# Performance work log

Measured on AMD Instinct MI355X. Metric: run time of the kernel, lower is better.

The kernel has to match this reference:

```python
import jax, jax.numpy as jnp
import numpy as np

B, S, D, H = 8, 1024, 768, 12
E = D // H  # head_size = 64
EPS = 1e-5


def _ln(x, g, b):
    mu = jnp.mean(x, axis=-1, keepdims=True)
    var = jnp.mean(jnp.square(x - mu), axis=-1, keepdims=True)
    return (x - mu) * jax.lax.rsqrt(var + EPS) * g + b


def setup_inputs() -> dict:
    key = jax.random.key(0)
    ks = jax.random.split(key, 16)
    w = lambda k, shape: jax.random.normal(k, shape, dtype=jnp.float32) * 0.02
    return {
        "x": jax.random.normal(ks[0], (B, S, D), dtype=jnp.float32),
        "ln1_g": jnp.ones((D,), jnp.float32),
        "ln1_b": jnp.zeros((D,), jnp.float32),
        "Wq": w(ks[1], (H, D, E)),
        "bq": w(ks[2], (H, E)),
        "Wv": w(ks[3], (H, D, E)),
        "bv": w(ks[4], (H, E)),
        "Wo": w(ks[5], (H * E, D)),
        "bo": w(ks[6], (D,)),
        "ln2_g": jnp.ones((D,), jnp.float32),
        "ln2_b": jnp.zeros((D,), jnp.float32),
        "W1": w(ks[7], (D, 4 * D)),
        "b1": w(ks[8], (4 * D,)),
        "W2": w(ks[9], (4 * D, D)),
        "b2": w(ks[10], (D,)),
    }


def reference(x, ln1_g, ln1_b, Wq, bq, Wv, bv, Wo, bo, ln2_g, ln2_b, W1, b1, W2, b2):
    d_k = x.shape[-1]
    h = _ln(x, ln1_g, ln1_b)
    # Faithful quirk: keys use the QUERY projection (k = self.query(x) in source).
    q = jnp.einsum('bsd,hde->bhse', h, Wq) + bq[None, :, None, :]
    k = q  # same projection, same input -> identical tensor
    v = jnp.einsum('bsd,hde->bhse', h, Wv) + bv[None, :, None, :]
    # Faithful quirk: scale uses full d_k, not head_size.
    scores = jnp.einsum('bhse,bhte->bhst', q, k) * (d_k ** -0.5)
    prob = jax.nn.softmax(scores, axis=-1)
    o = jnp.einsum('bhst,bhte->bhse', prob, v)  # [B,H,S,E]
    o = o.transpose(0, 2, 1, 3).reshape(x.shape[0], x.shape[1], -1)  # concat heads
    x = x + o @ Wo + bo
    h2 = _ln(x, ln2_g, ln2_b)
    mlp = jax.nn.gelu(h2 @ W1 + b1, approximate=False) @ W2 + b2
    return x + mlp
```

## Files before the change

### kernel.cpp

```cpp
#include <hip/hip_runtime.h>
#include <stdint.h>


typedef __attribute__((ext_vector_type(8))) short s8v;
typedef __attribute__((ext_vector_type(4))) float f32x4;
typedef __attribute__((ext_vector_type(4))) unsigned short us4v;

__device__ __forceinline__ unsigned short f2b(float f) {
  union { float f; unsigned u; } v; v.f = f;
  unsigned r = v.u + 0x7FFFu + ((v.u >> 16) & 1u);
  return (unsigned short)(r >> 16);
}

__device__ __forceinline__ void g2l16(const unsigned short* g, unsigned short* l) {
  __builtin_amdgcn_global_load_lds(
      (const __attribute__((address_space(1))) unsigned int*)g,
      (__attribute__((address_space(3))) unsigned int*)l, 16, 0, 0);
}

#define QSCALE 0.22816534f

__global__ __launch_bounds__(256) void repack_kernel(
    const float* __restrict__ Wq, const float* __restrict__ bq,
    const float* __restrict__ Wv, const float* __restrict__ bv,
    const float* __restrict__ Wo, const float* __restrict__ W1,
    const float* __restrict__ W2,
    unsigned short* __restrict__ Wqv_t, float* __restrict__ bias_qv,
    unsigned short* __restrict__ Wo_t, unsigned short* __restrict__ W1_t,
    unsigned short* __restrict__ W2_t)
{
  int i = blockIdx.x * 256 + threadIdx.x;
  if (i < 1536 * 768) {
    int n = i / 768, d = i % 768;
    float val;
    if (n < 768) { int h = n >> 6, e = n & 63; val = Wq[(h * 768 + d) * 64 + e] * QSCALE; }
    else { int c = n - 768; int h = c >> 6, e = c & 63; val = Wv[(h * 768 + d) * 64 + e]; }
    Wqv_t[i] = f2b(val);
  }
  if (i < 1536) bias_qv[i] = (i < 768) ? bq[i] * QSCALE : bv[i - 768];
  if (i < 768 * 768)  { int n = i / 768,  k = i % 768;  Wo_t[i] = f2b(Wo[k * 768  + n]); }
  if (i < 3072 * 768) { int n = i / 768,  k = i % 768;  W1_t[i] = f2b(W1[k * 3072 + n]); }
  if (i < 768 * 3072) { int n = i / 3072, k = i % 3072; W2_t[i] = f2b(W2[k * 768  + n]); }
}

__global__ __launch_bounds__(256) void ln_kernel(
    const float* __restrict__ x, const float* __restrict__ g,
    const float* __restrict__ b, unsigned short* __restrict__ out)
{
  __shared__ float red[4], red2[4];
  int row = blockIdx.x, t = threadIdx.x;
  const float* xr = x + (size_t)row * 768;
  float v0 = xr[t], v1 = xr[t + 256], v2 = xr[t + 512];
  float s = v0 + v1 + v2;
  #pragma unroll
  for (int m = 32; m; m >>= 1) s += __shfl_xor(s, m);
  if ((t & 63) == 0) red[t >> 6] = s;
  __syncthreads();
  float mean = (red[0] + red[1] + red[2] + red[3]) * (1.f / 768.f);
  float d0 = v0 - mean, d1 = v1 - mean, d2 = v2 - mean;
  float vs = d0 * d0 + d1 * d1 + d2 * d2;
  #pragma unroll
  for (int m = 32; m; m >>= 1) vs += __shfl_xor(vs, m);
  if ((t & 63) == 0) red2[t >> 6] = vs;
  __syncthreads();
  float var = (red2[0] + red2[1] + red2[2] + red2[3]) * (1.f / 768.f);
  float rs = rsqrtf(var + 1e-5f);
  unsigned short* o = out + (size_t)row * 768;
  o[t]       = f2b(d0 * rs * g[t]       + b[t]);
  o[t + 256] = f2b(d1 * rs * g[t + 256] + b[t + 256]);
  o[t + 512] = f2b(d2 * rs * g[t + 512] + b[t + 512]);
}

template<int EPI, int N, int K>
__global__ __launch_bounds__(512, 4) void gemm128(
    const unsigned short* __restrict__ A, const unsigned short* __restrict__ Bt,
    const float* __restrict__ bias,
    const float* resid, float* out_f32,
    unsigned short* __restrict__ out_bf,
    unsigned short* __restrict__ q_out, unsigned short* __restrict__ vt_out)
{
  __shared__ __align__(16) unsigned short As_[2][8192];
  __shared__ __align__(16) unsigned short Bs_[2][8192];
  constexpr int NTN = N >> 7;
  constexpr int NT = K >> 6;
  int bid = blockIdx.x;
  int q8 = gridDim.x >> 3;
  int sb = (bid & 7) * q8 + (bid >> 3);
  int m0 = (sb / NTN) << 7, n0 = (sb % NTN) << 7;
  int t = threadIdx.x, lane = t & 63, w = t >> 6;
  int l15 = lane & 15, lg = lane >> 4;
  int wm = (w >> 2) << 6;
  int wn = (w & 3) << 5;
  int lrow = lane >> 3;
  int lxor = ((lane & 7) ^ lrow) << 3;
  const unsigned short* Abase = A + (size_t)m0 * K;
  const unsigned short* Bbase = Bt + (size_t)n0 * K;

  auto stage = [&](int buf, int tile) {
    int k0 = tile << 6;
    #pragma unroll
    for (int j = 0; j < 2; ++j) {
      int row = j * 64 + w * 8 + lrow;
      int doff = (j * 512 + w * 64) * 8;
      g2l16(&Abase[(size_t)row * K + k0 + lxor], &As_[buf][doff]);
      g2l16(&Bbase[(size_t)row * K + k0 + lxor], &Bs_[buf][doff]);
    }
  };

  f32x4 acc[4][2] = {};
  stage(0, 0);
  asm volatile("s_waitcnt vmcnt(0)" ::: "memory");
  __builtin_amdgcn_sched_barrier(0);
  __builtin_amdgcn_s_barrier();

  int cswz = (l15 & 7) << 3;
  for (int tt = 0; tt < NT; ++tt) {
    int cur = tt & 1;
    if (tt + 1 < NT) {
      stage(cur ^ 1, tt + 1);
      asm volatile("s_waitcnt vmcnt(4)" ::: "memory");
    } else {
      asm volatile("s_waitcnt vmcnt(0)" ::: "memory");
    }
    __builtin_amdgcn_sched_barrier(0);
    __builtin_amdgcn_s_barrier();
    __builtin_amdgcn_sched_barrier(0);
    const unsigned short* Ac = &As_[cur][0];
    const unsigned short* Bc = &Bs_[cur][0];
    #pragma unroll
    for (int kk = 0; kk < 2; ++kk) {
      s8v a[4], b[2];
      int col = (kk * 32 + lg * 8) ^ cswz;
      #pragma unroll
      for (int i = 0; i < 4; ++i)
        a[i] = *(const s8v*)&Ac[(wm + i * 16 + l15) * 64 + col];
      #pragma unroll
      for (int i = 0; i < 2; ++i)
        b[i] = *(const s8v*)&Bc[(wn + i * 16 + l15) * 64 + col];
      __builtin_amdgcn_s_setprio(1);
      #pragma unroll
      for (int mi = 0; mi < 4; ++mi)
        #pragma unroll
        for (int ni = 0; ni < 2; ++ni)
          acc[mi][ni] = __builtin_amdgcn_mfma_f32_16x16x32_bf16(a[mi], b[ni], acc[mi][ni], 0, 0, 0);
      __builtin_amdgcn_s_setprio(0);
    }
    if (tt + 1 < NT) {
      __builtin_amdgcn_sched_barrier(0);
      __builtin_amdgcn_s_barrier();
      __builtin_amdgcn_sched_barrier(0);
    }
  }
  #pragma unroll
  for (int mi = 0; mi < 4; ++mi) {
    #pragma unroll
    for (int ni = 0; ni < 2; ++ni) {
      int col = n0 + wn + ni * 16 + l15;
      float bs = bias[col];
      #pragma unroll
      for (int r = 0; r < 4; ++r) {
        int row = m0 + wm + mi * 16 + lg * 4 + r;
        float v = acc[mi][ni][r] + bs;
        if (EPI == 1) {
          out_f32[(size_t)row * N + col] = resid[(size_t)row * N + col] + v;
        } else if (EPI == 2) {
          float v2 = v * v;
          float z = v * fmaf(-0.10294202f, v2, -2.302026f);
          float e; asm("v_exp_f32 %0, %1" : "=v"(e) : "v"(z));
          float rcp; asm("v_rcp_f32 %0, %1" : "=v"(rcp) : "v"(e + 1.0f));
          out_bf[(size_t)row * N + col] = f2b(v * rcp);
        } else {
          if (col < 768) {
            q_out[(size_t)row * 768 + col] = f2b(v);
          } else {
            int c = col - 768; int hh = c >> 6, e = c & 63;
            int bb = row >> 10, s = row & 1023;
            vt_out[(((size_t)(bb * 12 + hh)) * 64 + e) * 1024 + s] = f2b(v);
          }
        }
      }
    }
  }
}

__global__ __launch_bounds__(256) void attn_kernel(
    const unsigned short* __restrict__ qk,
    const unsigned short* __restrict__ vt,
    unsigned short* __restrict__ o)
{
  __shared__ __align__(16) unsigned short Qs[128 * 64];
  __shared__ __align__(16) unsigned short Ks[2][64 * 64];
  __shared__ __align__(16) unsigned short Vs[2][64 * 64];
  __shared__ __align__(16) unsigned short Ps[128 * 64];
  int bid = blockIdx.x;
  int xcd = bid & 7, idx = bid >> 3;
  int bh = xcd * 12 + (idx >> 3), qt = idx & 7;
  int b = bh / 12, h = bh % 12;
  int t = threadIdx.x, lane = t & 63, w = t >> 6;
  int l15 = lane & 15, lg = lane >> 4;
  int wq0 = w << 5;
  size_t qrow0 = (size_t)b * 1024 + qt * 128;
  size_t krow0 = (size_t)b * 1024;
  size_t vbase = ((size_t)bh) * 64 * 1024;

  int srow = t >> 3;
  int scsw = ((t & 7) << 3) ^ ((srow & 7) << 3);
  const unsigned short* qsrc = &qk[(qrow0 + srow) * 768 + h * 64 + scsw];
  const unsigned short* ksrc = &qk[(krow0 + srow) * 768 + h * 64 + scsw];
  const unsigned short* vsrc = &vt[vbase + (size_t)srow * 1024 + scsw];

  #pragma unroll
  for (int j = 0; j < 4; ++j)
    g2l16(qsrc + (size_t)j * 32 * 768, &Qs[(j * 256 + w * 64) * 8]);
  #pragma unroll
  for (int j = 0; j < 2; ++j) {
    g2l16(ksrc + (size_t)j * 32 * 768, &Ks[0][(j * 256 + w * 64) * 8]);
    g2l16(vsrc + (size_t)j * 32 * 1024, &Vs[0][(j * 256 + w * 64) * 8]);
  }
  asm volatile("s_waitcnt vmcnt(0)" ::: "memory");
  __builtin_amdgcn_s_barrier();

  f32x4 oacc[4][2] = {};
  float lsum[2] = {0.f, 0.f};
  int cswz = (l15 & 7) << 3;

  for (int kt = 0; kt < 16; ++kt) {
    int buf = kt & 1;
    if (kt < 15) {
      const unsigned short* kp = ksrc + (size_t)(kt + 1) * 64 * 768;
      const unsigned short* vp = vsrc + (kt + 1) * 64;
      #pragma unroll
      for (int j = 0; j < 2; ++j) {
        g2l16(kp + (size_t)j * 32 * 768, &Ks[buf ^ 1][(j * 256 + w * 64) * 8]);
        g2l16(vp + (size_t)j * 32 * 1024, &Vs[buf ^ 1][(j * 256 + w * 64) * 8]);
      }
    }
    const unsigned short* Kb = Ks[buf];
    const unsigned short* Vb = Vs[buf];
    f32x4 st[4][2] = {};
    #pragma unroll
    for (int kk = 0; kk < 2; ++kk) {
      int col = (kk * 32 + lg * 8) ^ cswz;
      s8v a[4], bq2[2];
      #pragma unroll
      for (int i = 0; i < 4; ++i) a[i] = *(const s8v*)&Kb[(i * 16 + l15) * 64 + col];
      #pragma unroll
      for (int i = 0; i < 2; ++i) bq2[i] = *(const s8v*)&Qs[(wq0 + i * 16 + l15) * 64 + col];
      #pragma unroll
      for (int mi = 0; mi < 4; ++mi)
        #pragma unroll
        for (int ni = 0; ni < 2; ++ni)
          st[mi][ni] = __builtin_amdgcn_mfma_f32_16x16x32_bf16(a[mi], bq2[ni], st[mi][ni], 0, 0, 0);
    }
    #pragma unroll
    for (int ni = 0; ni < 2; ++ni) {
      int prow = (wq0 + ni * 16 + l15) * 64;
      #pragma unroll
      for (int mi = 0; mi < 4; ++mi) {
        float p0, p1, p2, p3;
        asm("v_exp_f32 %0, %1" : "=v"(p0) : "v"(st[mi][ni][0]));
        asm("v_exp_f32 %0, %1" : "=v"(p1) : "v"(st[mi][ni][1]));
        asm("v_exp_f32 %0, %1" : "=v"(p2) : "v"(st[mi][ni][2]));
        asm("v_exp_f32 %0, %1" : "=v"(p3) : "v"(st[mi][ni][3]));
        lsum[ni] += (p0 + p1) + (p2 + p3);
        unsigned lo, hi;
        asm("v_cvt_pk_bf16_f32 %0, %1, %2" : "=v"(lo) : "v"(p0), "v"(p1));
        asm("v_cvt_pk_bf16_f32 %0, %1, %2" : "=v"(hi) : "v"(p2), "v"(p3));
        unsigned long long pk = (unsigned long long)lo | ((unsigned long long)hi << 32);
        *(unsigned long long*)&Ps[prow + ((mi * 16 + lg * 4) ^ cswz)] = pk;
      }
    }
    #pragma unroll
    for (int kk = 0; kk < 2; ++kk) {
      int col = (kk * 32 + lg * 8) ^ cswz;
      s8v a[4], bp[2];
      #pragma unroll
      for (int i = 0; i < 4; ++i) a[i] = *(const s8v*)&Vb[(i * 16 + l15) * 64 + col];
      #pragma unroll
      for (int i = 0; i < 2; ++i) bp[i] = *(const s8v*)&Ps[(wq0 + i * 16 + l15) * 64 + col];
      #pragma unroll
      for (int ei = 0; ei < 4; ++ei)
        #pragma unroll
        for (int ni = 0; ni < 2; ++ni)
          oacc[ei][ni] = __builtin_amdgcn_mfma_f32_16x16x32_bf16(a[ei], bp[ni], oacc[ei][ni], 0, 0, 0);
    }
    asm volatile("s_waitcnt vmcnt(0)" ::: "memory");
    __builtin_amdgcn_s_barrier();
  }
  #pragma unroll
  for (int ni = 0; ni < 2; ++ni) {
    float s = lsum[ni];
    s += __shfl_xor(s, 16);
    s += __shfl_xor(s, 32);
    float inv = 1.f / s;
    int q = wq0 + ni * 16 + l15;
    size_t obase = (qrow0 + q) * 768 + h * 64;
    #pragma unroll
    for (int ei = 0; ei < 4; ++ei) {
      us4v ov;
      #pragma unroll
      for (int r = 0; r < 4; ++r) ov[r] = f2b(oacc[ei][ni][r] * inv);
      *(us4v*)&o[obase + ei * 16 + lg * 4] = ov;
    }
  }
}

extern "C" void kernel_launch(void* const* d_in, const int* in_sizes, int n_in,
                              void* d_out, int out_size, void* d_ws, size_t ws_size,
                              hipStream_t stream)
{
  const float* x     = (const float*)d_in[0];
  const float* ln1_g = (const float*)d_in[1];
  const float* ln1_b = (const float*)d_in[2];
  const float* Wq    = (const float*)d_in[3];
  const float* bq    = (const float*)d_in[4];
  const float* Wv    = (const float*)d_in[5];
  const float* bv    = (const float*)d_in[6];
  const float* Wo    = (const float*)d_in[7];
  const float* bo    = (const float*)d_in[8];
  const float* ln2_g = (const float*)d_in[9];
  const float* ln2_b = (const float*)d_in[10];
  const float* W1    = (const float*)d_in[11];
  const float* b1    = (const float*)d_in[12];
  const float* W2    = (const float*)d_in[13];
  const float* b2    = (const float*)d_in[14];
  float* out = (float*)d_out;

  char* ws = (char*)d_ws;
  size_t off = 0;
  auto alloc = [&](size_t bytes) -> void* {
    void* p = ws + off; off += (bytes + 255) & ~(size_t)255; return p;
  };
  unsigned short* Wqv_t  = (unsigned short*)alloc(1536ull * 768 * 2);
  float*          bias_qv= (float*)         alloc(1536ull * 4);
  unsigned short* Wo_t   = (unsigned short*)alloc(768ull * 768 * 2);
  unsigned short* W1_t   = (unsigned short*)alloc(3072ull * 768 * 2);
  unsigned short* W2_t   = (unsigned short*)alloc(768ull * 3072 * 2);
  unsigned short* h_bf   = (unsigned short*)alloc(8192ull * 768 * 2);
  unsigned short* q_bf   = (unsigned short*)alloc(8192ull * 768 * 2);
  unsigned short* v_t    = (unsigned short*)alloc(96ull * 64 * 1024 * 2);
  unsigned short* o_bf   = (unsigned short*)alloc(8192ull * 768 * 2);
  unsigned short* h2_bf  = (unsigned short*)alloc(8192ull * 768 * 2);
  unsigned short* m1_bf  = (unsigned short*)alloc(8192ull * 3072 * 2);

  repack_kernel<<<9216, 256, 0, stream>>>(Wq, bq, Wv, bv, Wo, W1, W2,
                                          Wqv_t, bias_qv, Wo_t, W1_t, W2_t);
  ln_kernel<<<8192, 256, 0, stream>>>(x, ln1_g, ln1_b, h_bf);
  gemm128<3, 1536, 768><<<768, 512, 0, stream>>>(h_bf, Wqv_t, bias_qv,
      nullptr, nullptr, nullptr, q_bf, v_t);
  attn_kernel<<<768, 256, 0, stream>>>(q_bf, v_t, o_bf);
  gemm128<1, 768, 768><<<384, 512, 0, stream>>>(o_bf, Wo_t, bo,
      x, out, nullptr, nullptr, nullptr);
  ln_kernel<<<8192, 256, 0, stream>>>(out, ln2_g, ln2_b, h2_bf);
  gemm128<2, 3072, 768><<<1536, 512, 0, stream>>>(h2_bf, W1_t, b1,
      nullptr, nullptr, m1_bf, nullptr, nullptr);
  gemm128<1, 768, 3072><<<384, 512, 0, stream>>>(m1_bf, W2_t, b2,
      out, out, nullptr, nullptr, nullptr);
}
```

Before: 278.3 us.

## Split K across wave pairs in GEMM with LDS reduction of partial accumulators

The 128x128 GEMM now assigns each group of four waves a 64x64 output sub-tile and splits the 64-wide K tile between two wave groups, each handling 32. Each wave loads 4 A and 4 B fragments for 16 MFMAs per tile instead of 4+2 fragments for 8 MFMAs over two k-steps. This raises MFMA-to-LDS-read ratio. After the main loop, the upper four waves write their partial sums into LDS, and the lower four add them and run the epilogue. The cost is doubled accumulator registers, an extra reduction with two barriers, and an epilogue executed by only half the waves.

Result: slower. 299.3 us (median of 2 runs) (+7.5%).

```diff
diff --git a/kernel.cpp b/kernel.cpp
--- a/kernel.cpp
+++ b/kernel.cpp
@@ -79,8 +79,7 @@
     unsigned short* __restrict__ out_bf,
     unsigned short* __restrict__ q_out, unsigned short* __restrict__ vt_out)
 {
-  __shared__ __align__(16) unsigned short As_[2][8192];
-  __shared__ __align__(16) unsigned short Bs_[2][8192];
+  __shared__ __align__(16) unsigned short SMEM[2][16384];
   constexpr int NTN = N >> 7;
   constexpr int NT = K >> 6;
   int bid = blockIdx.x;
@@ -89,8 +88,8 @@
   int m0 = (sb / NTN) << 7, n0 = (sb % NTN) << 7;
   int t = threadIdx.x, lane = t & 63, w = t >> 6;
   int l15 = lane & 15, lg = lane >> 4;
-  int wm = (w >> 2) << 6;
-  int wn = (w & 3) << 5;
+  int p = w & 3, kks = w >> 2;
+  int wm = (p >> 1) << 6, wn = (p & 1) << 6;
   int lrow = lane >> 3;
   int lxor = ((lane & 7) ^ lrow) << 3;
   const unsigned short* Abase = A + (size_t)m0 * K;
@@ -102,18 +101,18 @@
     for (int j = 0; j < 2; ++j) {
       int row = j * 64 + w * 8 + lrow;
       int doff = (j * 512 + w * 64) * 8;
-      g2l16(&Abase[(size_t)row * K + k0 + lxor], &As_[buf][doff]);
-      g2l16(&Bbase[(size_t)row * K + k0 + lxor], &Bs_[buf][doff]);
+      g2l16(&Abase[(size_t)row * K + k0 + lxor], &SMEM[buf][doff]);
+      g2l16(&Bbase[(size_t)row * K + k0 + lxor], &SMEM[buf][8192 + doff]);
     }
   };
 
-  f32x4 acc[4][2] = {};
+  f32x4 acc[4][4] = {};
   stage(0, 0);
   asm volatile("s_waitcnt vmcnt(0)" ::: "memory");
   __builtin_amdgcn_sched_barrier(0);
   __builtin_amdgcn_s_barrier();
 
-  int cswz = (l15 & 7) << 3;
+  int col = (kks * 32 + lg * 8) ^ ((l15 & 7) << 3);
   for (int tt = 0; tt < NT; ++tt) {
     int cur = tt & 1;
     if (tt + 1 < NT) {
@@ -125,57 +124,72 @@
     __builtin_amdgcn_sched_barrier(0);
     __builtin_amdgcn_s_barrier();
     __builtin_amdgcn_sched_barrier(0);
-    const unsigned short* Ac = &As_[cur][0];
-    const unsigned short* Bc = &Bs_[cur][0];
-    #pragma unroll
-    for (int kk = 0; kk < 2; ++kk) {
-      s8v a[4], b[2];
-      int col = (kk * 32 + lg * 8) ^ cswz;
-      #pragma unroll
-      for (int i = 0; i < 4; ++i)
-        a[i] = *(const s8v*)&Ac[(wm + i * 16 + l15) * 64 + col];
-      #pragma unroll
-      for (int i = 0; i < 2; ++i)
-        b[i] = *(const s8v*)&Bc[(wn + i * 16 + l15) * 64 + col];
-      __builtin_amdgcn_s_setprio(1);
-      #pragma unroll
-      for (int mi = 0; mi < 4; ++mi)
-        #pragma unroll
-        for (int ni = 0; ni < 2; ++ni)
-          acc[mi][ni] = __builtin_amdgcn_mfma_f32_16x16x32_bf16(a[mi], b[ni], acc[mi][ni], 0, 0, 0);
-      __builtin_amdgcn_s_setprio(0);
-    }
+    const unsigned short* Ac = &SMEM[cur][0];
+    const unsigned short* Bc = &SMEM[cur][8192];
+    s8v a[4], b[4];
+    #pragma unroll
+    for (int i = 0; i < 4; ++i)
+      a[i] = *(const s8v*)&Ac[(wm + i * 16 + l15) * 64 + col];
+    #pragma unroll
+    for (int i = 0; i < 4; ++i)
+      b[i] = *(const s8v*)&Bc[(wn + i * 16 + l15) * 64 + col];
+    __builtin_amdgcn_s_setprio(1);
+    #pragma unroll
+    for (int mi = 0; mi < 4; ++mi)
+      #pragma unroll
+      for (int ni = 0; ni < 4; ++ni)
+        acc[mi][ni] = __builtin_amdgcn_mfma_f32_16x16x32_bf16(a[mi], b[ni], acc[mi][ni], 0, 0, 0);
+    __builtin_amdgcn_s_setprio(0);
     if (tt + 1 < NT) {
       __builtin_amdgcn_sched_barrier(0);
       __builtin_amdgcn_s_barrier();
       __builtin_amdgcn_sched_barrier(0);
     }
   }
-  #pragma unroll
-  for (int mi = 0; mi < 4; ++mi) {
-    #pragma unroll
-    for (int ni = 0; ni < 2; ++ni) {
-      int col = n0 + wn + ni * 16 + l15;
-      float bs = bias[col];
-      #pragma unroll
-      for (int r = 0; r < 4; ++r) {
-        int row = m0 + wm + mi * 16 + lg * 4 + r;
-        float v = acc[mi][ni][r] + bs;
-        if (EPI == 1) {
-          out_f32[(size_t)row * N + col] = resid[(size_t)row * N + col] + v;
-        } else if (EPI == 2) {
-          float v2 = v * v;
-          float z = v * fmaf(-0.10294202f, v2, -2.302026f);
-          float e; asm("v_exp_f32 %0, %1" : "=v"(e) : "v"(z));
-          float rcp; asm("v_rcp_f32 %0, %1" : "=v"(rcp) : "v"(e + 1.0f));
-          out_bf[(size_t)row * N + col] = f2b(v * rcp);
-        } else {
-          if (col < 768) {
-            q_out[(size_t)row * 768 + col] = f2b(v);
+  __syncthreads();
+  float* red = (float*)&SMEM[0][0];
+  if (w >= 4) {
+    #pragma unroll
+    for (int mi = 0; mi < 4; ++mi)
+      #pragma unroll
+      for (int ni = 0; ni < 4; ++ni)
+        *(f32x4*)&red[(w - 4) * 4096 + (mi * 4 + ni) * 256 + lane * 4] = acc[mi][ni];
+  }
+  __syncthreads();
+  if (w < 4) {
+    #pragma unroll
+    for (int mi = 0; mi < 4; ++mi)
+      #pragma unroll
+      for (int ni = 0; ni < 4; ++ni) {
+        f32x4 o = *(const f32x4*)&red[w * 4096 + (mi * 4 + ni) * 256 + lane * 4];
+        acc[mi][ni] += o;
+      }
+    #pragma unroll
+    for (int mi = 0; mi < 4; ++mi) {
+      #pragma unroll
+      for (int ni = 0; ni < 4; ++ni) {
+        int colo = n0 + wn + ni * 16 + l15;
+        float bs = bias[colo];
+        #pragma unroll
+        for (int r = 0; r < 4; ++r) {
+          int row = m0 + wm + mi * 16 + lg * 4 + r;
+          float v = acc[mi][ni][r] + bs;
+          if (EPI == 1) {
+            out_f32[(size_t)row * N + colo] = resid[(size_t)row * N + colo] + v;
+          } else if (EPI == 2) {
+            float v2 = v * v;
+            float z = v * fmaf(-0.10294202f, v2, -2.302026f);
+            float e; asm("v_exp_f32 %0, %1" : "=v"(e) : "v"(z));
+            float rcp; asm("v_rcp_f32 %0, %1" : "=v"(rcp) : "v"(e + 1.0f));
+            out_bf[(size_t)row * N + colo] = f2b(v * rcp);
           } else {
-            int c = col - 768; int hh = c >> 6, e = c & 63;
-            int bb = row >> 10, s = row & 1023;
-            vt_out[(((size_t)(bb * 12 + hh)) * 64 + e) * 1024 + s] = f2b(v);
+            if (colo < 768) {
+              q_out[(size_t)row * 768 + colo] = f2b(v);
+            } else {
+              int c = colo - 768; int hh = c >> 6, e = c & 63;
+              int bb = row >> 10, s = row & 1023;
+              vt_out[(((size_t)(bb * 12 + hh)) * 64 + e) * 1024 + s] = f2b(v);
+            }
           }
         }
       }
```

## Use 128x64 tile GEMM for final W2 projection to double block count

Applied to the files above, without the earlier changes.

Adds a new GEMM kernel with a 128x64 output tile, double-buffered LDS loads and an XOR swizzle, and uses it for the W2 down-projection (N=768, K=3072). This launches 768 blocks instead of 384 so the compute units are better filled on a GEMM whose output is narrow. In exchange each block reuses loaded A data across fewer output columns, so A traffic rises and each wave does a smaller MFMA tile.

New measurement: 270.7 us. -2.7%, faster.

```diff
diff --git a/kernel.cpp b/kernel.cpp
--- a/kernel.cpp
+++ b/kernel.cpp
@@ -183,6 +183,99 @@
   }
 }
 
+template<int N, int K>
+__global__ __launch_bounds__(512, 6) void gemm_n64(
+    const unsigned short* __restrict__ A, const unsigned short* __restrict__ Bt,
+    const float* __restrict__ bias, const float* resid, float* out_f32)
+{
+  __shared__ __align__(16) unsigned short As_[2][8192];
+  __shared__ __align__(16) unsigned short Bs_[2][4096];
+  constexpr int NTN = N >> 6;
+  constexpr int NT = K >> 6;
+  int bid = blockIdx.x;
+  int q8 = gridDim.x >> 3;
+  int sb = (bid & 7) * q8 + (bid >> 3);
+  int m0 = (sb / NTN) << 7, n0 = (sb % NTN) << 6;
+  int t = threadIdx.x, lane = t & 63, w = t >> 6;
+  int l15 = lane & 15, lg = lane >> 4;
+  int wm = (w >> 1) << 5;
+  int wn = (w & 1) << 5;
+  int lrow = lane >> 3;
+  int lxor = ((lane & 7) ^ lrow) << 3;
+  const unsigned short* Abase = A + (size_t)m0 * K;
+  const unsigned short* Bbase = Bt + (size_t)n0 * K;
+
+  auto stage = [&](int buf, int tile) {
+    int k0 = tile << 6;
+    #pragma unroll
+    for (int j = 0; j < 2; ++j) {
+      int row = j * 64 + w * 8 + lrow;
+      g2l16(&Abase[(size_t)row * K + k0 + lxor], &As_[buf][(j * 512 + w * 64) * 8]);
+    }
+    int brow = w * 8 + lrow;
+    g2l16(&Bbase[(size_t)brow * K + k0 + lxor], &Bs_[buf][w * 512]);
+  };
+
+  f32x4 acc[2][2] = {};
+  stage(0, 0);
+  asm volatile("s_waitcnt vmcnt(0)" ::: "memory");
+  __builtin_amdgcn_sched_barrier(0);
+  __builtin_amdgcn_s_barrier();
+
+  int cswz = (l15 & 7) << 3;
+  for (int tt = 0; tt < NT; ++tt) {
+    int cur = tt & 1;
+    if (tt + 1 < NT) {
+      stage(cur ^ 1, tt + 1);
+      asm volatile("s_waitcnt vmcnt(3)" ::: "memory");
+    } else {
+      asm volatile("s_waitcnt vmcnt(0)" ::: "memory");
+    }
+    __builtin_amdgcn_sched_barrier(0);
+    __builtin_amdgcn_s_barrier();
+    __builtin_amdgcn_sched_barrier(0);
+    const unsigned short* Ac = &As_[cur][0];
+    const unsigned short* Bc = &Bs_[cur][0];
+    #pragma unroll
+    for (int kk = 0; kk < 2; ++kk) {
+      s8v a[2], b[2];
+      int col = (kk * 32 + lg * 8) ^ cswz;
+      #pragma unroll
+      for (int i = 0; i < 2; ++i)
+        a[i] = *(const s8v*)&Ac[(wm + i * 16 + l15) * 64 + col];
+      #pragma unroll
+      for (int i = 0; i < 2; ++i)
+        b[i] = *(const s8v*)&Bc[(wn + i * 16 + l15) * 64 + col];
+      __builtin_amdgcn_s_setprio(1);
+      #pragma unroll
+      for (int mi = 0; mi < 2; ++mi)
+        #pragma unroll
+        for (int ni = 0; ni < 2; ++ni)
+          acc[mi][ni] = __builtin_amdgcn_mfma_f32_16x16x32_bf16(a[mi], b[ni], acc[mi][ni], 0, 0, 0);
+      __builtin_amdgcn_s_setprio(0);
+    }
+    if (tt + 1 < NT) {
+      __builtin_amdgcn_sched_barrier(0);
+      __builtin_amdgcn_s_barrier();
+      __builtin_amdgcn_sched_barrier(0);
+    }
+  }
+  #pragma unroll
+  for (int mi = 0; mi < 2; ++mi) {
+    #pragma unroll
+    for (int ni = 0; ni < 2; ++ni) {
+      int col = n0 + wn + ni * 16 + l15;
+      float bs = bias[col];
+      #pragma unroll
+      for (int r = 0; r < 4; ++r) {
+        int row = m0 + wm + mi * 16 + lg * 4 + r;
+        float v = acc[mi][ni][r] + bs;
+        out_f32[(size_t)row * N + col] = resid[(size_t)row * N + col] + v;
+      }
+    }
+  }
+}
+
 __global__ __launch_bounds__(256) void attn_kernel(
     const unsigned short* __restrict__ qk,
     const unsigned short* __restrict__ vt,
@@ -354,6 +447,5 @@
   ln_kernel<<<8192, 256, 0, stream>>>(out, ln2_g, ln2_b, h2_bf);
   gemm128<2, 3072, 768><<<1536, 512, 0, stream>>>(h2_bf, W1_t, b1,
       nullptr, nullptr, m1_bf, nullptr, nullptr);
-  gemm128<1, 768, 3072><<<384, 512, 0, stream>>>(m1_bf, W2_t, b2,
-      out, out, nullptr, nullptr, nullptr);
-}
+  gemm_n64<768, 3072><<<768, 512, 0, stream>>>(m1_bf, W2_t, b2, out, out);
+}
```
